# Performance work log

Measured on AMD Instinct MI355X. Metric: run time of the kernel, lower is better.

## Reference

```python
import jax, jax.numpy as jnp
import numpy as np

B, S, D, H = 2, 2048, 1024, 16
DH = D // H
NEG = -1000000000.0


def setup_inputs() -> dict:
    key = jax.random.key(0)
    ks = jax.random.split(key, 8)
    q = jax.random.normal(ks[0], (B, S, D), dtype=jnp.float32)
    k = jax.random.normal(ks[1], (B, S, D), dtype=jnp.float32)
    v = jax.random.normal(ks[2], (B, S, D), dtype=jnp.float32)
    # padding mask [B, k_len]; ensure first key position is valid
    mask = jax.random.randint(ks[3], (B, S), 0, 2, dtype=jnp.int32)
    mask = mask.at[:, 0].set(1)
    scale = 1.0 / np.sqrt(D)
    Wq = jax.random.normal(ks[4], (D, D), dtype=jnp.float32) * scale
    Wk = jax.random.normal(ks[5], (D, D), dtype=jnp.float32) * scale
    Wv = jax.random.normal(ks[6], (D, D), dtype=jnp.float32) * scale
    Wo = jax.random.normal(ks[7], (D, D), dtype=jnp.float32) * scale
    return {"q": q, "k": k, "v": v, "mask": mask,
            "Wq": Wq, "Wk": Wk, "Wv": Wv, "Wo": Wo}


def reference(q, k, v, mask, Wq, Wk, Wv, Wo):
    # nn.Linear(bias=False): y = x @ W.T  (W is [out, in])
    Q = jnp.einsum('bsd,ed->bse', q, Wq)
    K = jnp.einsum('bsd,ed->bse', k, Wk)
    V = jnp.einsum('bsd,ed->bse', v, Wv)
    # split heads -> [B, H, S, DH]
    Q = Q.reshape(B, S, H, DH).transpose(0, 2, 1, 3)
    K = K.reshape(B, S, H, DH).transpose(0, 2, 1, 3)
    V = V.reshape(B, S, H, DH).transpose(0, 2, 1, 3)
    scores = jnp.einsum('bhqd,bhkd->bhqk', Q, K) / jnp.float32(np.sqrt(DH))
    # padding mask: [B, K] -> additive [B, 1, 1, K]
    pad = jnp.where(mask == 0, jnp.float32(NEG), jnp.float32(0.0))[:, None, None, :]
    scores = scores + pad
    # causal (mask_future=True): strict upper triangle blocked
    causal = jnp.where(jnp.triu(jnp.ones((S, S), dtype=bool), k=1),
                       jnp.float32(NEG), jnp.float32(0.0))
    scores = scores + causal
    attn = jax.nn.softmax(scores, axis=-1)
    out = jnp.einsum('bhqk,bhkd->bhqd', attn, V)  # [B, H, S, DH]
    out = out.transpose(0, 2, 1, 3).reshape(B, S, D)
    out = jnp.einsum('bsd,ed->bse', out, Wo)
    # dropout: identity in eval mode
    return out
```

## Files before the change

kernel.cpp:

```cpp
#include <hip/hip_runtime.h>
#include <stdint.h>

#define BB 2
#define SS 2048
#define DD 1024
#define HH 16
#define DHH 64

typedef __bf16 bf16_t;
typedef bf16_t bf16x8 __attribute__((ext_vector_type(8)));
typedef float f32x4 __attribute__((ext_vector_type(4)));
typedef short s16x4 __attribute__((ext_vector_type(4)));

union FragU { uint4 u; bf16x8 b; };
union Frag4U { uint2 u; s16x4 s; };

#if __has_builtin(__builtin_amdgcn_exp2f)
#define EXP2(x) __builtin_amdgcn_exp2f(x)
#else
#define EXP2(x) exp2f(x)
#endif

__device__ __forceinline__ unsigned short f2bf(float f) {
  union { float f; unsigned int u; } x; x.f = f;
  unsigned int u = x.u;
  return (unsigned short)((u + 0x7FFFu + ((u >> 16) & 1u)) >> 16);
}

__device__ __forceinline__ uint2 pack4(float4 v) {
  uint2 r;
  r.x = (unsigned)f2bf(v.x) | ((unsigned)f2bf(v.y) << 16);
  r.y = (unsigned)f2bf(v.z) | ((unsigned)f2bf(v.w) << 16);
  return r;
}

__device__ __forceinline__ uint2 packAcc(f32x4 a) {
  uint2 r;
  r.x = (unsigned)f2bf(a[0]) | ((unsigned)f2bf(a[1]) << 16);
  r.y = (unsigned)f2bf(a[2]) | ((unsigned)f2bf(a[3]) << 16);
  return r;
}

__device__ __forceinline__ bf16x8 ldsFrag(const unsigned short* s, int idx) {
  FragU f;
  f.u = *reinterpret_cast<const uint4*>(s + idx);
  return f.b;
}

__device__ __forceinline__ void gload_lds16(const unsigned short* g, unsigned short* s) {
  __builtin_amdgcn_global_load_lds(
      (const __attribute__((address_space(1))) unsigned int*)g,
      (__attribute__((address_space(3))) unsigned int*)s, 16, 0, 0);
}

#define MFMA16(a, b, c) __builtin_amdgcn_mfma_f32_16x16x32_bf16((a), (b), (c), 0, 0, 0)
#define MFMA16K16(a, b, c) __builtin_amdgcn_mfma_f32_16x16x16bf16_1k((a), (b), (c), 0, 0, 0)

__global__ __launch_bounds__(256) void convert_kernel(
    const float* __restrict__ q, const float* __restrict__ k, const float* __restrict__ v,
    const float* __restrict__ Wq, const float* __restrict__ Wk,
    const float* __restrict__ Wv, const float* __restrict__ Wo,
    const int* __restrict__ mask,
    unsigned short* __restrict__ Ab, unsigned short* __restrict__ Wb,
    float* __restrict__ Mf) {
  const int z = blockIdx.y;
  if (z == 7) {
    if (blockIdx.x >= 4) return;
    const size_t base = (size_t)blockIdx.x * 1024 + (size_t)threadIdx.x * 4;
    int4 m4 = *reinterpret_cast<const int4*>(mask + base);
    float4 p;
    p.x = (m4.x == 0) ? -1.0e9f : 0.0f;
    p.y = (m4.y == 0) ? -1.0e9f : 0.0f;
    p.z = (m4.z == 0) ? -1.0e9f : 0.0f;
    p.w = (m4.w == 0) ? -1.0e9f : 0.0f;
    *reinterpret_cast<float4*>(Mf + base) = p;
    return;
  }
  const float* src;
  unsigned short* dst;
  float scale = 1.0f;
  if (z < 3) {
    src = (z == 0) ? q : (z == 1) ? k : v;
    dst = Ab + (size_t)z * BB * SS * DD;
  } else {
    if (blockIdx.x >= (DD * DD / 1024)) return;
    src = (z == 3) ? Wq : (z == 4) ? Wk : (z == 5) ? Wv : Wo;
    dst = Wb + (size_t)(z - 3) * DD * DD;
    if (z == 3) scale = 0.125f * 1.44269504088896f;
  }
  const size_t base = (size_t)blockIdx.x * 1024 + (size_t)threadIdx.x * 4;
  float4 val = *reinterpret_cast<const float4*>(src + base);
  val.x *= scale; val.y *= scale; val.z *= scale; val.w *= scale;
  uint2 p = pack4(val);
  *reinterpret_cast<uint2*>(dst + base) = p;
}

__global__ __launch_bounds__(256) void proj128_kernel(
    const unsigned short* __restrict__ Ab, const unsigned short* __restrict__ Wb,
    unsigned short* __restrict__ Qb, unsigned short* __restrict__ Kb,
    unsigned short* __restrict__ Vt) {
  __shared__ unsigned short sA[2][128 * 64];
  __shared__ unsigned short sB[2][128 * 64];

  const int z = blockIdx.z;
  const unsigned short* A = Ab + (size_t)z * BB * SS * DD;
  const unsigned short* W = Wb + (size_t)z * DD * DD;
  unsigned short* Out = (z == 0) ? Qb : (z == 1) ? Kb : Vt;
  const int layout = (z == 2) ? 1 : 0;

  const int t = threadIdx.x;
  const int lane = t & 63, wave = t >> 6;
  const int quad = lane >> 4, l15 = lane & 15;
  const int wr = wave >> 1, wc = wave & 1;
  const int mBase = blockIdx.x * 128, nBase = blockIdx.y * 128;
  const int srow = lane >> 3, soct = lane & 7;

  f32x4 acc[4][4] = {};

  #pragma unroll
  for (int i = 0; i < 4; ++i) {
    const int g = wave * 4 + i;
    const int row = g * 8 + srow;
    const int oct = soct ^ (row & 7);
    gload_lds16(A + (size_t)(mBase + row) * DD + oct * 8, &sA[0][g * 512]);
    gload_lds16(W + (size_t)(nBase + row) * DD + oct * 8, &sB[0][g * 512]);
  }

  for (int kt = 0; kt < DD / 64; ++kt) {
    __syncthreads();
    if (kt + 1 < DD / 64) {
      const int nb = (kt + 1) & 1;
      const int k1 = (kt + 1) * 64;
      #pragma unroll
      for (int i = 0; i < 4; ++i) {
        const int g = wave * 4 + i;
        const int row = g * 8 + srow;
        const int oct = soct ^ (row & 7);
        gload_lds16(A + (size_t)(mBase + row) * DD + k1 + oct * 8, &sA[nb][g * 512]);
        gload_lds16(W + (size_t)(nBase + row) * DD + k1 + oct * 8, &sB[nb][g * 512]);
      }
    }
    const int cb = kt & 1;
    #pragma unroll
    for (int kk = 0; kk < 2; ++kk) {
      bf16x8 af[4], bfr[4];
      #pragma unroll
      for (int i = 0; i < 4; ++i) {
        const int row = wr * 64 + i * 16 + l15;
        af[i] = ldsFrag(sA[cb], (row * 8 + ((kk * 4 + quad) ^ (l15 & 7))) * 8);
      }
      #pragma unroll
      for (int j = 0; j < 4; ++j) {
        const int row = wc * 64 + j * 16 + l15;
        bfr[j] = ldsFrag(sB[cb], (row * 8 + ((kk * 4 + quad) ^ (l15 & 7))) * 8);
      }
      if (layout == 0) {
        #pragma unroll
        for (int i = 0; i < 4; ++i)
          #pragma unroll
          for (int j = 0; j < 4; ++j)
            acc[i][j] = MFMA16(bfr[j], af[i], acc[i][j]);
      } else {
        #pragma unroll
        for (int i = 0; i < 4; ++i)
          #pragma unroll
          for (int j = 0; j < 4; ++j)
            acc[i][j] = MFMA16(af[i], bfr[j], acc[i][j]);
      }
    }
  }

  const int b = mBase >> 11;
  const int sbase = mBase & (SS - 1);
  if (layout == 0) {
    #pragma unroll
    for (int i = 0; i < 4; ++i) {
      #pragma unroll
      for (int j = 0; j < 4; ++j) {
        const int s = sbase + wr * 64 + i * 16 + l15;
        const int n = nBase + wc * 64 + j * 16 + quad * 4;
        const int h = n >> 6, dh = n & (DHH - 1);
        uint2 w = packAcc(acc[i][j]);
        *reinterpret_cast<uint2*>(
            Out + ((size_t)(b * HH + h) * SS + s) * DHH + dh) = w;
      }
    }
  } else {
    #pragma unroll
    for (int i = 0; i < 4; ++i) {
      #pragma unroll
      for (int j = 0; j < 4; ++j) {
        const int s = sbase + wr * 64 + i * 16 + quad * 4;
        const int n = nBase + wc * 64 + j * 16 + l15;
        const int h = n >> 6, dh = n & (DHH - 1);
        uint2 w = packAcc(acc[i][j]);
        *reinterpret_cast<uint2*>(
            Out + ((size_t)(b * HH + h) * DHH + dh) * SS + s) = w;
      }
    }
  }
}

__global__ __launch_bounds__(256, 4) void attn_kernel(
    const unsigned short* __restrict__ Qb, const unsigned short* __restrict__ Kb,
    const unsigned short* __restrict__ Vt, const float* __restrict__ Mf,
    unsigned short* __restrict__ Obh) {
  __shared__ __align__(16) unsigned short sK[2][64 * 64];
  __shared__ __align__(16) unsigned short sV[2][64 * 64];
  unsigned short* sO = &sK[0][0];

  const int t = threadIdx.x;
  const int lane = t & 63, wave = t >> 6;
  const int quad = lane >> 4, l15 = lane & 15;

  const int id = blockIdx.x;
  const int xcd = id & 7, rest = id >> 3;
  const int hg = rest >> 5;
  const int hd = xcd * 4 + hg;
  const int r5 = rest & 31;
  const int qt = (hg & 1) ? (31 - r5) : r5;
  const int b = hd >> 4;
  const int qb = qt * 64;

  const size_t headOff = (size_t)hd * SS * DHH;
  const unsigned short* Qh = Qb + headOff;
  const unsigned short* Kh = Kb + headOff;
  const unsigned short* Vh = Vt + headOff;
  const float* Mp = Mf + b * SS;

  bf16x8 aq[2];
  {
    const unsigned short* qp = Qh + (size_t)(qb + wave * 16 + l15) * DHH + quad * 8;
    FragU f0, f1;
    f0.u = *reinterpret_cast<const uint4*>(qp);
    f1.u = *reinterpret_cast<const uint4*>(qp + 32);
    aq[0] = f0.b; aq[1] = f1.b;
  }

  const int srow = lane >> 3, soct = lane & 7;

  #pragma unroll
  for (int i = 0; i < 2; ++i) {
    const int g = wave * 2 + i;
    const int row = g * 8 + srow;
    const int oct = soct ^ (row & 7);
    gload_lds16(Kh + (size_t)row * DHH + oct * 8, &sK[0][g * 512]);
    gload_lds16(Vh + (size_t)row * SS + oct * 8, &sV[0][g * 512]);
  }

  float m_l = -1.0e30f, l_l = 0.0f;
  f32x4 oacc[4] = {};
  const int qrow_abs = qb + wave * 16 + l15;

  for (int c = 0; c <= qt; ++c) {
    __syncthreads();
    if (c < qt) {
      const int c1 = (c + 1) * 64;
      const int nb = (c + 1) & 1;
      #pragma unroll
      for (int i = 0; i < 2; ++i) {
        const int g = wave * 2 + i;
        const int row = g * 8 + srow;
        const int oct = soct ^ (row & 7);
        gload_lds16(Kh + (size_t)(c1 + row) * DHH + oct * 8, &sK[nb][g * 512]);
        gload_lds16(Vh + (size_t)row * SS + c1 + oct * 8, &sV[nb][g * 512]);
      }
    }
    const int cb = c & 1;
    const int c0 = c * 64;

    f32x4 sacc[4] = {};
    #pragma unroll
    for (int kk = 0; kk < 2; ++kk) {
      #pragma unroll
      for (int j = 0; j < 4; ++j) {
        const int row = j * 16 + l15;
        bf16x8 ak = ldsFrag(sK[cb], (row * 8 + ((kk * 4 + quad) ^ (l15 & 7))) * 8);
        sacc[j] = MFMA16(ak, aq[kk], sacc[j]);
      }
    }

    float rm = -1.0e30f;
    #pragma unroll
    for (int j = 0; j < 4; ++j)
      rm = fmaxf(rm, fmaxf(fmaxf(sacc[j][0], sacc[j][1]), fmaxf(sacc[j][2], sacc[j][3])));
    rm = fmaxf(rm, __shfl_xor(rm, 16));
    rm = fmaxf(rm, __shfl_xor(rm, 32));
    const float mnew = fmaxf(m_l, rm);
    const float alpha = EXP2(m_l - mnew);
    m_l = mnew;

    const bool diag = (c == qt);
    float rs = 0.0f;
    s16x4 pk[4];
    #pragma unroll
    for (int j = 0; j < 4; ++j) {
      float4 pf = *reinterpret_cast<const float4*>(Mp + c0 + j * 16 + quad * 4);
      float p0 = EXP2(sacc[j][0] - mnew + pf.x);
      float p1 = EXP2(sacc[j][1] - mnew + pf.y);
      float p2 = EXP2(sacc[j][2] - mnew + pf.z);
      float p3 = EXP2(sacc[j][3] - mnew + pf.w);
      if (diag) {
        const int key = c0 + j * 16 + quad * 4;
        p0 = (key + 0 > qrow_abs) ? 0.0f : p0;
        p1 = (key + 1 > qrow_abs) ? 0.0f : p1;
        p2 = (key + 2 > qrow_abs) ? 0.0f : p2;
        p3 = (key + 3 > qrow_abs) ? 0.0f : p3;
      }
      rs += (p0 + p1) + (p2 + p3);
      Frag4U fu;
      fu.u.x = __builtin_amdgcn_perm(__float_as_uint(p1) + 0x8000u,
                                     __float_as_uint(p0) + 0x8000u, 0x07060302u);
      fu.u.y = __builtin_amdgcn_perm(__float_as_uint(p3) + 0x8000u,
                                     __float_as_uint(p2) + 0x8000u, 0x07060302u);
      pk[j] = fu.s;
    }
    rs += __shfl_xor(rs, 16);
    rs += __shfl_xor(rs, 32);
    l_l = l_l * alpha + rs;

    #pragma unroll
    for (int jn = 0; jn < 4; ++jn)
      oacc[jn] *= alpha;

    #pragma unroll
    for (int j = 0; j < 4; ++j) {
      #pragma unroll
      for (int jn = 0; jn < 4; ++jn) {
        const int row = jn * 16 + l15;
        const int oct = (2 * j + (quad >> 1)) ^ (l15 & 7);
        Frag4U av;
        av.u = *reinterpret_cast<const uint2*>(&sV[cb][(row * 8 + oct) * 8 + (quad & 1) * 4]);
        oacc[jn] = MFMA16K16(av.s, pk[j], oacc[jn]);
      }
    }
  }

  __syncthreads();
  const float inv = 1.0f / l_l;
  #pragma unroll
  for (int jn = 0; jn < 4; ++jn) {
    uint2 w;
    w.x = (unsigned)f2bf(oacc[jn][0] * inv) | ((unsigned)f2bf(oacc[jn][1] * inv) << 16);
    w.y = (unsigned)f2bf(oacc[jn][2] * inv) | ((unsigned)f2bf(oacc[jn][3] * inv) << 16);
    *reinterpret_cast<uint2*>(&sO[(wave * 16 + l15) * 72 + jn * 16 + quad * 4]) = w;
  }
  __syncthreads();
  {
    const int row = t >> 2, seg = t & 3;
    uint4 u0 = *reinterpret_cast<const uint4*>(&sO[row * 72 + seg * 16]);
    uint4 u1 = *reinterpret_cast<const uint4*>(&sO[row * 72 + seg * 16 + 8]);
    unsigned short* dst = Obh + headOff + (size_t)(qb + row) * DHH + seg * 16;
    *reinterpret_cast<uint4*>(dst) = u0;
    *reinterpret_cast<uint4*>(dst + 8) = u1;
  }
}

__global__ __launch_bounds__(256) void outproj_kernel(
    const unsigned short* __restrict__ Obh, const unsigned short* __restrict__ Wb,
    float* __restrict__ Out) {
  __shared__ unsigned short sA[2][128 * 64];
  __shared__ unsigned short sB[2][128 * 64];

  const unsigned short* W = Wb + (size_t)3 * DD * DD;
  const int t = threadIdx.x;
  const int lane = t & 63, wave = t >> 6;
  const int quad = lane >> 4, l15 = lane & 15;
  const int wr = wave >> 1, wc = wave & 1;
  const int mBase = blockIdx.x * 128, nBase = blockIdx.y * 128;
  const int srow = lane >> 3, soct = lane & 7;

  const int bidx = mBase >> 11;
  const int sloc = mBase & (SS - 1);
  const unsigned short* Abase = Obh + (size_t)bidx * HH * SS * DHH;

  f32x4 acc[4][4] = {};

  #pragma unroll
  for (int i = 0; i < 4; ++i) {
    const int g = wave * 4 + i;
    const int row = g * 8 + srow;
    const int oct = soct ^ (row & 7);
    gload_lds16(Abase + ((size_t)0 * SS + sloc + row) * DHH + oct * 8, &sA[0][g * 512]);
    gload_lds16(W + (size_t)(nBase + row) * DD + oct * 8, &sB[0][g * 512]);
  }

  for (int kt = 0; kt < HH; ++kt) {
    __syncthreads();
    if (kt + 1 < HH) {
      const int nb = (kt + 1) & 1;
      #pragma unroll
      for (int i = 0; i < 4; ++i) {
        const int g = wave * 4 + i;
        const int row = g * 8 + srow;
        const int oct = soct ^ (row & 7);
        gload_lds16(Abase + ((size_t)(kt + 1) * SS + sloc + row) * DHH + oct * 8,
                    &sA[nb][g * 512]);
        gload_lds16(W + (size_t)(nBase + row) * DD + (kt + 1) * 64 + oct * 8,
                    &sB[nb][g * 512]);
      }
    }
    const int cb = kt & 1;
    #pragma unroll
    for (int kk = 0; kk < 2; ++kk) {
      bf16x8 af[4], bfr[4];
      #pragma unroll
      for (int i = 0; i < 4; ++i) {
        const int row = wr * 64 + i * 16 + l15;
        af[i] = ldsFrag(sA[cb], (row * 8 + ((kk * 4 + quad) ^ (l15 & 7))) * 8);
      }
      #pragma unroll
      for (int j = 0; j < 4; ++j) {
        const int row = wc * 64 + j * 16 + l15;
        bfr[j] = ldsFrag(sB[cb], (row * 8 + ((kk * 4 + quad) ^ (l15 & 7))) * 8);
      }
      #pragma unroll
      for (int i = 0; i < 4; ++i)
        #pragma unroll
        for (int j = 0; j < 4; ++j)
          acc[i][j] = MFMA16(bfr[j], af[i], acc[i][j]);
    }
  }

  #pragma unroll
  for (int i = 0; i < 4; ++i) {
    #pragma unroll
    for (int j = 0; j < 4; ++j) {
      const int m = mBase + wr * 64 + i * 16 + l15;
      const int n = nBase + wc * 64 + j * 16 + quad * 4;
      float4 w;
      w.x = acc[i][j][0]; w.y = acc[i][j][1];
      w.z = acc[i][j][2]; w.w = acc[i][j][3];
      *reinterpret_cast<float4*>(Out + (size_t)m * DD + n) = w;
    }
  }
}

extern "C" void kernel_launch(void* const* d_in, const int* in_sizes, int n_in,
                              void* d_out, int out_size, void* d_ws, size_t ws_size,
                              hipStream_t stream) {
  (void)in_sizes; (void)n_in; (void)out_size; (void)ws_size;
  const float* q  = (const float*)d_in[0];
  const float* k  = (const float*)d_in[1];
  const float* v  = (const float*)d_in[2];
  const int* mask = (const int*)d_in[3];
  const float* Wq = (const float*)d_in[4];
  const float* Wk = (const float*)d_in[5];
  const float* Wv = (const float*)d_in[6];
  const float* Wo = (const float*)d_in[7];
  float* out = (float*)d_out;

  const size_t AE = (size_t)BB * SS * DD;
  unsigned short* Ab  = (unsigned short*)d_ws;
  unsigned short* Obh = Ab;
  unsigned short* Wb  = Ab + 3 * AE;
  unsigned short* Qb  = Wb + (size_t)4 * DD * DD;
  unsigned short* Kb  = Qb + AE;
  unsigned short* Vt  = Kb + AE;
  float* Mf = (float*)(Vt + AE);

  convert_kernel<<<dim3(AE / 1024, 8), 256, 0, stream>>>(
      q, k, v, Wq, Wk, Wv, Wo, mask, Ab, Wb, Mf);

  proj128_kernel<<<dim3(BB * SS / 128, DD / 128, 3), 256, 0, stream>>>(
      Ab, Wb, Qb, Kb, Vt);

  attn_kernel<<<dim3(32 * HH * BB), 256, 0, stream>>>(Qb, Kb, Vt, Mf, Obh);

  outproj_kernel<<<dim3(BB * SS / 128, DD / 128), 256, 0, stream>>>(Obh, Wb, out);
}
```

Measured before the change: 220.7 us.

## Split long causal attention rows across two blocks with a combine kernel

Query tiles 16..31 are split into two key-range halves handled by separate blocks, which write unnormalized partial outputs plus running max and sum to workspace. A new combine kernel merges the halves using log-sum-exp weights and writes bf16 output. Short tiles still finish in one block. The aim is to balance the triangular causal workload and raise block count from 1024 to 1536. In exchange it adds fp32 partial traffic and an extra kernel launch.

```diff
diff --git a/kernel.cpp b/kernel.cpp
--- a/kernel.cpp
+++ b/kernel.cpp
@@ -204,7 +204,8 @@
 __global__ __launch_bounds__(256, 4) void attn_kernel(
     const unsigned short* __restrict__ Qb, const unsigned short* __restrict__ Kb,
     const unsigned short* __restrict__ Vt, const float* __restrict__ Mf,
-    unsigned short* __restrict__ Obh) {
+    unsigned short* __restrict__ Obh, float* __restrict__ PO,
+    float* __restrict__ PM) {
   __shared__ __align__(16) unsigned short sK[2][64 * 64];
   __shared__ __align__(16) unsigned short sV[2][64 * 64];
   unsigned short* sO = &sK[0][0];
@@ -215,10 +216,17 @@
 
   const int id = blockIdx.x;
   const int xcd = id & 7, rest = id >> 3;
-  const int hg = rest >> 5;
+  const int w = rest >> 2, hg = rest & 3;
   const int hd = xcd * 4 + hg;
-  const int r5 = rest & 31;
-  const int qt = (hg & 1) ? (31 - r5) : r5;
+  int qt, cBeg, cEnd, half;
+  if (w < 16)       { qt = 16 + w; cBeg = 0;  cEnd = 16;     half = 0;  }
+  else if (w == 16) { qt = 15;     cBeg = 0;  cEnd = 16;     half = -1; }
+  else if (w == 17) { qt = 31;     cBeg = 16; cEnd = 32;     half = 1;  }
+  else {
+    const int p = (w - 18) >> 1;
+    if (((w - 18) & 1) == 0) { qt = 14 - p; cBeg = 0;  cEnd = qt + 1; half = -1; }
+    else                     { qt = 30 - p; cBeg = 16; cEnd = qt + 1; half = 1;  }
+  }
   const int b = hd >> 4;
   const int qb = qt * 64;
 
@@ -239,22 +247,25 @@
 
   const int srow = lane >> 3, soct = lane & 7;
 
-  #pragma unroll
-  for (int i = 0; i < 2; ++i) {
-    const int g = wave * 2 + i;
-    const int row = g * 8 + srow;
-    const int oct = soct ^ (row & 7);
-    gload_lds16(Kh + (size_t)row * DHH + oct * 8, &sK[0][g * 512]);
-    gload_lds16(Vh + (size_t)row * SS + oct * 8, &sV[0][g * 512]);
+  {
+    const int cb0 = cBeg * 64;
+    #pragma unroll
+    for (int i = 0; i < 2; ++i) {
+      const int g = wave * 2 + i;
+      const int row = g * 8 + srow;
+      const int oct = soct ^ (row & 7);
+      gload_lds16(Kh + (size_t)(cb0 + row) * DHH + oct * 8, &sK[0][g * 512]);
+      gload_lds16(Vh + (size_t)row * SS + cb0 + oct * 8, &sV[0][g * 512]);
+    }
   }
 
   float m_l = -1.0e30f, l_l = 0.0f;
   f32x4 oacc[4] = {};
   const int qrow_abs = qb + wave * 16 + l15;
 
-  for (int c = 0; c <= qt; ++c) {
+  for (int c = cBeg; c < cEnd; ++c) {
     __syncthreads();
-    if (c < qt) {
+    if (c + 1 < cEnd) {
       const int c1 = (c + 1) * 64;
       const int nb = (c + 1) & 1;
       #pragma unroll
@@ -336,21 +347,80 @@
     }
   }
 
+  if (half < 0) {
+    __syncthreads();
+    const float inv = 1.0f / l_l;
+    #pragma unroll
+    for (int jn = 0; jn < 4; ++jn) {
+      uint2 wv;
+      wv.x = (unsigned)f2bf(oacc[jn][0] * inv) | ((unsigned)f2bf(oacc[jn][1] * inv) << 16);
+      wv.y = (unsigned)f2bf(oacc[jn][2] * inv) | ((unsigned)f2bf(oacc[jn][3] * inv) << 16);
+      *reinterpret_cast<uint2*>(&sO[(wave * 16 + l15) * 72 + jn * 16 + quad * 4]) = wv;
+    }
+    __syncthreads();
+    {
+      const int row = t >> 2, seg = t & 3;
+      uint4 u0 = *reinterpret_cast<const uint4*>(&sO[row * 72 + seg * 16]);
+      uint4 u1 = *reinterpret_cast<const uint4*>(&sO[row * 72 + seg * 16 + 8]);
+      unsigned short* dst = Obh + headOff + (size_t)(qb + row) * DHH + seg * 16;
+      *reinterpret_cast<uint4*>(dst) = u0;
+      *reinterpret_cast<uint4*>(dst + 8) = u1;
+    }
+  } else {
+    const int pIdx2 = (hd * 16 + (qt - 16)) * 2 + half;
+    float* po = PO + (size_t)pIdx2 * 4096;
+    #pragma unroll
+    for (int jn = 0; jn < 4; ++jn) {
+      #pragma unroll
+      for (int r = 0; r < 4; ++r) {
+        const int dh = jn * 16 + quad * 4 + r;
+        po[dh * 64 + wave * 16 + l15] = oacc[jn][r];
+      }
+    }
+    if (quad == 0) {
+      float* pm = PM + (size_t)pIdx2 * 128;
+      pm[wave * 16 + l15] = m_l;
+      pm[64 + wave * 16 + l15] = l_l;
+    }
+  }
+}
+
+__global__ __launch_bounds__(256) void combine_kernel(
+    const float* __restrict__ PO, const float* __restrict__ PM,
+    unsigned short* __restrict__ Obh) {
+  __shared__ float sml[256];
+  __shared__ unsigned short sO[64 * 72];
+  const int t = threadIdx.x;
+  const int pIdx = blockIdx.x;
+  const int hd = pIdx >> 4, qt = 16 + (pIdx & 15);
+  const float* p0 = PO + ((size_t)pIdx * 2 + 0) * 4096;
+  const float* p1 = PO + ((size_t)pIdx * 2 + 1) * 4096;
+  const float* pm0 = PM + ((size_t)pIdx * 2 + 0) * 128;
+  const float* pm1 = PM + ((size_t)pIdx * 2 + 1) * 128;
+  if (t < 128) sml[t] = pm0[t];
+  else sml[t] = pm1[t - 128];
   __syncthreads();
-  const float inv = 1.0f / l_l;
+
+  const int row = t >> 2;
+  const int seg = t & 3;
   #pragma unroll
-  for (int jn = 0; jn < 4; ++jn) {
-    uint2 w;
-    w.x = (unsigned)f2bf(oacc[jn][0] * inv) | ((unsigned)f2bf(oacc[jn][1] * inv) << 16);
-    w.y = (unsigned)f2bf(oacc[jn][2] * inv) | ((unsigned)f2bf(oacc[jn][3] * inv) << 16);
-    *reinterpret_cast<uint2*>(&sO[(wave * 16 + l15) * 72 + jn * 16 + quad * 4]) = w;
+  for (int i = 0; i < 16; ++i) {
+    const int q = seg * 16 + i;
+    const float m1 = sml[q], l1 = sml[64 + q];
+    const float m2 = sml[128 + q], l2 = sml[192 + q];
+    const float mm = fmaxf(m1, m2);
+    const float w1 = EXP2(m1 - mm), w2 = EXP2(m2 - mm);
+    const float inv = 1.0f / (l1 * w1 + l2 * w2);
+    const float o = (p0[row * 64 + q] * w1 + p1[row * 64 + q] * w2) * inv;
+    sO[q * 72 + row] = f2bf(o);
   }
   __syncthreads();
   {
-    const int row = t >> 2, seg = t & 3;
-    uint4 u0 = *reinterpret_cast<const uint4*>(&sO[row * 72 + seg * 16]);
-    uint4 u1 = *reinterpret_cast<const uint4*>(&sO[row * 72 + seg * 16 + 8]);
-    unsigned short* dst = Obh + headOff + (size_t)(qb + row) * DHH + seg * 16;
+    const int r2 = t >> 2, s2 = t & 3;
+    uint4 u0 = *reinterpret_cast<const uint4*>(&sO[r2 * 72 + s2 * 16]);
+    uint4 u1 = *reinterpret_cast<const uint4*>(&sO[r2 * 72 + s2 * 16 + 8]);
+    unsigned short* dst = Obh + (size_t)hd * SS * DHH +
+                          (size_t)(qt * 64 + r2) * DHH + s2 * 16;
     *reinterpret_cast<uint4*>(dst) = u0;
     *reinterpret_cast<uint4*>(dst + 8) = u1;
   }
@@ -453,11 +523,13 @@
   const size_t AE = (size_t)BB * SS * DD;
   unsigned short* Ab  = (unsigned short*)d_ws;
   unsigned short* Obh = Ab;
+  float* PO = (float*)(Ab + AE);
   unsigned short* Wb  = Ab + 3 * AE;
   unsigned short* Qb  = Wb + (size_t)4 * DD * DD;
   unsigned short* Kb  = Qb + AE;
   unsigned short* Vt  = Kb + AE;
   float* Mf = (float*)(Vt + AE);
+  float* PM = Mf + (size_t)BB * SS;
 
   convert_kernel<<<dim3(AE / 1024, 8), 256, 0, stream>>>(
       q, k, v, Wq, Wk, Wv, Wo, mask, Ab, Wb, Mf);
@@ -465,7 +537,8 @@
   proj128_kernel<<<dim3(BB * SS / 128, DD / 128, 3), 256, 0, stream>>>(
       Ab, Wb, Qb, Kb, Vt);
 
-  attn_kernel<<<dim3(32 * HH * BB), 256, 0, stream>>>(Qb, Kb, Vt, Mf, Obh);
+  attn_kernel<<<dim3(48 * HH * BB), 256, 0, stream>>>(Qb, Kb, Vt, Mf, Obh, PO, PM);
+  combine_kernel<<<dim3(512), 256, 0, stream>>>(PO, PM, Obh);
 
   outproj_kernel<<<dim3(BB * SS / 128, DD / 128), 256, 0, stream>>>(Obh, Wb, out);
 }
```

Measured after the change: 224.9 us. About the same (+1.9%).
